# Kernel tuning notes

Hardware: AMD Instinct MI355X
Metric: run time of the kernel (lower is better)

The kernel has to match this reference:

```python
import jax, jax.numpy as jnp
import numpy as np

D_MODEL = 1024
NUM_HEADS = 16
D_IN = 1024

def setup_inputs() -> dict:
    key = jax.random.key(0)
    ks = jax.random.split(key, 5)
    scale = 1.0 / np.sqrt(D_IN)
    return {
        "in_features": jax.random.normal(ks[0], (4, 2048, D_IN), dtype=jnp.float32),
        "q_weight": jax.random.normal(ks[1], (D_MODEL, D_IN), dtype=jnp.float32) * scale,
        "k_weight": jax.random.normal(ks[2], (D_MODEL, D_IN), dtype=jnp.float32) * scale,
        "v_weight": jax.random.normal(ks[3], (D_MODEL, D_IN), dtype=jnp.float32) * scale,
        "o_weight": jax.random.normal(ks[4], (D_MODEL, D_MODEL), dtype=jnp.float32) * scale,
    }

def reference(in_features, q_weight, k_weight, v_weight, o_weight):
    batch, seq_len, _ = in_features.shape
    d_head = D_MODEL // NUM_HEADS
    # QKV projections (Linear with no bias: x @ W^T)
    q = jnp.einsum('bsi,di->bsd', in_features, q_weight)
    k = jnp.einsum('bsi,di->bsd', in_features, k_weight)
    v = jnp.einsum('bsi,di->bsd', in_features, v_weight)
    # split heads -> [b, h, s, d_head]
    q = q.reshape(batch, seq_len, NUM_HEADS, d_head).transpose(0, 2, 1, 3)
    k = k.reshape(batch, seq_len, NUM_HEADS, d_head).transpose(0, 2, 1, 3)
    v = v.reshape(batch, seq_len, NUM_HEADS, d_head).transpose(0, 2, 1, 3)
    # scaled dot-product attention (scale by per-head dim, as in SelfAttention)
    scores = jnp.einsum('bhqd,bhkd->bhqk', q, k) / jnp.sqrt(jnp.float32(d_head))
    probs = jax.nn.softmax(scores, axis=-1)
    ctx = jnp.einsum('bhqk,bhkd->bhqd', probs, v)
    # merge heads -> [b, s, d_model]
    ctx = ctx.transpose(0, 2, 1, 3).reshape(batch, seq_len, D_MODEL)
    # output projection
    return jnp.einsum('bsd,md->bsm', ctx, o_weight)
```

## Files before the change

kernel.cpp:

```cpp
#include <hip/hip_runtime.h>

typedef _Float16 half8 __attribute__((ext_vector_type(8)));
typedef _Float16 half4v __attribute__((ext_vector_type(4)));
typedef __fp16 fp16x2 __attribute__((ext_vector_type(2)));
typedef float f32x4 __attribute__((ext_vector_type(4)));
typedef float f32x16 __attribute__((ext_vector_type(16)));

__device__ __forceinline__ void gload_lds16(const _Float16* g, _Float16* l) {
    __builtin_amdgcn_global_load_lds(
        (const __attribute__((address_space(1))) void*)g,
        (__attribute__((address_space(3))) void*)l,
        16, 0, 0);
}

__global__ void cvt_f32_f16(const float* __restrict__ src, _Float16* __restrict__ dst, int n4) {
    int i = blockIdx.x * blockDim.x + threadIdx.x;
    if (i >= n4) return;
    f32x4 v = ((const f32x4*)src)[i];
    half4v h;
    h[0] = (_Float16)v[0]; h[1] = (_Float16)v[1];
    h[2] = (_Float16)v[2]; h[3] = (_Float16)v[3];
    ((half4v*)dst)[i] = h;
}

__global__ void cvt4_f32_f16(const float* __restrict__ s0, const float* __restrict__ s1,
                             const float* __restrict__ s2, const float* __restrict__ s3,
                             _Float16* __restrict__ dst) {
    int i = blockIdx.x * blockDim.x + threadIdx.x;
    int wsel = blockIdx.y;
    const float* src = (wsel == 0) ? s0 : (wsel == 1) ? s1 : (wsel == 2) ? s2 : s3;
    f32x4 v = ((const f32x4*)src)[i];
    half4v h;
    h[0] = (_Float16)v[0]; h[1] = (_Float16)v[1];
    h[2] = (_Float16)v[2]; h[3] = (_Float16)v[3];
    ((half4v*)(dst + (size_t)wsel * 1048576))[i] = h;
}

template<int MODE>
__global__ __launch_bounds__(256, 2)
void gemm_nt(const _Float16* __restrict__ A,
             const _Float16* __restrict__ Wbase,
             void* __restrict__ outbase)
{
    __shared__ _Float16 lds[32768];
    _Float16* Asb = lds;
    _Float16* Bsb = lds + 16384;

    const int tid  = threadIdx.x;
    const int lane = tid & 63;
    const int w    = tid >> 6;
    const int wr   = w >> 1, wc = w & 1;
    const int lr   = lane & 15, lg = lane >> 4;
    const int brow = blockIdx.x * 128;
    const int bcol = blockIdx.y * 128;
    const int mat  = (MODE == 0) ? blockIdx.z : 0;

    const _Float16* Ap = A + (size_t)brow * 1024;
    const _Float16* Bp = Wbase + (size_t)mat * (1024u * 1024u) + (size_t)bcol * 1024;

    const int srw  = tid >> 2;
    const int sch  = tid & 3;
    const int soff = ((sch ^ (srw & 3)) << 3);

    auto stage = [&](int buf, int kt) {
#pragma unroll
        for (int i = 0; i < 2; ++i) {
            const int ra = i * 64 + srw;
            gload_lds16(Ap + (size_t)ra * 1024 + kt * 32 + soff,
                        Asb + buf * 4096 + i * 2048 + w * 512);
            gload_lds16(Bp + (size_t)ra * 1024 + kt * 32 + soff,
                        Bsb + buf * 4096 + i * 2048 + w * 512);
        }
    };

    f32x4 acc[4][4] = {};
    const int swz = ((lg ^ (lr & 3)) << 3);

    stage(0, 0);
    stage(1, 1);
    asm volatile("s_waitcnt vmcnt(4)" ::: "memory");
    __builtin_amdgcn_s_barrier();
    __builtin_amdgcn_sched_barrier(0);

    for (int t = 0; t < 32; ++t) {
        if (t < 30) stage((t + 2) & 3, t + 2);
        const _Float16* Ab = Asb + (t & 3) * 4096;
        const _Float16* Bb = Bsb + (t & 3) * 4096;
        half8 af[4], bf[4];
#pragma unroll
        for (int mi = 0; mi < 4; ++mi)
            af[mi] = *(const half8*)&Ab[(wr * 64 + mi * 16 + lr) * 32 + swz];
#pragma unroll
        for (int ni = 0; ni < 4; ++ni)
            bf[ni] = *(const half8*)&Bb[(wc * 64 + ni * 16 + lr) * 32 + swz];
        __builtin_amdgcn_s_setprio(1);
#pragma unroll
        for (int mi = 0; mi < 4; ++mi)
#pragma unroll
            for (int ni = 0; ni < 4; ++ni)
                acc[mi][ni] = __builtin_amdgcn_mfma_f32_16x16x32_f16(af[mi], bf[ni], acc[mi][ni], 0, 0, 0);
        __builtin_amdgcn_s_setprio(0);
        if (t < 30)       { asm volatile("s_waitcnt vmcnt(4)" ::: "memory"); }
        else if (t == 30) { asm volatile("s_waitcnt vmcnt(0)" ::: "memory"); }
        if (t < 31) {
            __builtin_amdgcn_s_barrier();
            __builtin_amdgcn_sched_barrier(0);
        }
    }

    if (MODE == 0) {
        _Float16* outp = (_Float16*)outbase + (size_t)mat * (8192u * 1024u);
        if (mat == 2) {
            _Float16* Ts = lds;
#pragma unroll
            for (int p = 0; p < 2; ++p) {
                __syncthreads();
                if (wc == p) {
#pragma unroll
                    for (int mi = 0; mi < 4; ++mi)
#pragma unroll
                        for (int ni = 0; ni < 4; ++ni) {
                            int drow = ni * 16 + lr;
                            int s0   = wr * 64 + mi * 16 + lg * 4;
                            half4v o;
#pragma unroll
                            for (int r = 0; r < 4; ++r) o[r] = (_Float16)acc[mi][ni][r];
                            int byteoff = drow * 256 + s0 * 2;
                            byteoff ^= (drow & 7) << 4;
                            *(half4v*)((char*)Ts + byteoff) = o;
                        }
                }
                __syncthreads();
                {
                    int row   = tid >> 2;
                    int cbase = (tid & 3) * 4;
                    int gd = bcol + p * 64 + row;
                    int h = gd >> 6, dd = gd & 63;
                    int b = brow >> 11, sseq = brow & 2047;
                    _Float16* gout = outp + (((size_t)b * 16 + h) * 64 + dd) * 2048 + sseq;
#pragma unroll
                    for (int j = 0; j < 4; ++j) {
                        int c  = cbase + j;
                        int lc = c ^ (row & 7);
                        half8 v = *(const half8*)&Ts[row * 128 + lc * 8];
                        *(half8*)&gout[c * 8] = v;
                    }
                }
            }
        } else {
            const float scale = (mat == 0) ? 0.18033688f : 1.0f;
#pragma unroll
            for (int mi = 0; mi < 4; ++mi)
#pragma unroll
                for (int ni = 0; ni < 4; ++ni)
#pragma unroll
                    for (int r = 0; r < 4; ++r) {
                        int row = brow + wr * 64 + mi * 16 + lg * 4 + r;
                        int col = bcol + wc * 64 + ni * 16 + lr;
                        int b = row >> 11, s = row & 2047;
                        int h = col >> 6,  d = col & 63;
                        outp[(((size_t)b * 16 + h) * 2048 + s) * 64 + d] =
                            (_Float16)(acc[mi][ni][r] * scale);
                    }
        }
    } else {
        float* outp = (float*)outbase;
#pragma unroll
        for (int mi = 0; mi < 4; ++mi)
#pragma unroll
            for (int ni = 0; ni < 4; ++ni)
#pragma unroll
                for (int r = 0; r < 4; ++r) {
                    int row = brow + wr * 64 + mi * 16 + lg * 4 + r;
                    int col = bcol + wc * 64 + ni * 16 + lr;
                    outp[(size_t)row * 1024 + col] = acc[mi][ni][r];
                }
    }
}

#define M_FIX 10.0f
__global__ __launch_bounds__(256, 2)
void attn_kernel(const _Float16* __restrict__ Q,
                 const _Float16* __restrict__ Kx,
                 const _Float16* __restrict__ Vt,
                 _Float16* __restrict__ Ctx)
{
    __shared__ _Float16 Ks[2][64 * 72];
    __shared__ _Float16 Vs[2][64 * 72];

    const int tid = threadIdx.x, lane = tid & 63, w = tid >> 6;
    const int l31 = lane & 31, hi = lane >> 5;

    const int wg = blockIdx.x;
    const int j = ((wg & 7) << 6) + (wg >> 3);
    const int bh = j >> 3, qblk = j & 7;

    const _Float16* Qp  = Q  + ((size_t)bh * 2048 + qblk * 256) * 64;
    const _Float16* Kp  = Kx + (size_t)bh * 2048 * 64;
    const _Float16* Vtp = Vt + (size_t)bh * 64 * 2048;

    half8 qf[2][4];
#pragma unroll
    for (int g = 0; g < 2; ++g)
#pragma unroll
        for (int ks = 0; ks < 4; ++ks)
            qf[g][ks] = *(const half8*)(Qp + (size_t)(w * 64 + g * 32 + l31) * 64 + ks * 16 + hi * 8);

    const int srow = tid >> 3;
    const int scol = (tid & 7) * 8;
    const _Float16* Kg0 = Kp  + (size_t)srow * 64   + scol;
    const _Float16* Vg0 = Vtp + (size_t)srow * 2048 + scol;
    const int ldso = srow * 72 + scol;

    const fp16x2 ones2 = {(__fp16)1.0f, (__fp16)1.0f};

    f32x16 cacc[2][2] = {};
    float lp[2][2] = {};

    half8 kr0, kr1, vr0, vr1;
    kr0 = *(const half8*)(Kg0);
    kr1 = *(const half8*)(Kg0 + 2048);
    vr0 = *(const half8*)(Vg0);
    vr1 = *(const half8*)(Vg0 + 32 * 2048);
    *(half8*)&Ks[0][ldso]           = kr0;
    *(half8*)&Ks[0][ldso + 32 * 72] = kr1;
    *(half8*)&Vs[0][ldso]           = vr0;
    *(half8*)&Vs[0][ldso + 32 * 72] = vr1;
    __syncthreads();

    for (int t = 0; t < 32; ++t) {
        const int cur = t & 1;
        if (t < 31) {
            kr0 = *(const half8*)(Kg0 + (size_t)(t + 1) * 4096);
            kr1 = *(const half8*)(Kg0 + (size_t)(t + 1) * 4096 + 2048);
        }

        f32x16 sf[2][2];
        __builtin_amdgcn_s_setprio(1);
#pragma unroll
        for (int g = 0; g < 2; ++g)
#pragma unroll
            for (int kt = 0; kt < 2; ++kt) {
                f32x16 z;
#pragma unroll
                for (int r = 0; r < 16; ++r) z[r] = -M_FIX;
#pragma unroll
                for (int ks = 0; ks < 4; ++ks) {
                    half8 kf = *(const half8*)&Ks[cur][(kt * 32 + l31) * 72 + ks * 16 + hi * 8];
                    z = __builtin_amdgcn_mfma_f32_32x32x16_f16(kf, qf[g][ks], z, 0, 0, 0);
                }
                sf[g][kt] = z;
            }
        __builtin_amdgcn_s_setprio(0);

        if (t < 31) {
            *(half8*)&Ks[cur ^ 1][ldso]           = kr0;
            *(half8*)&Ks[cur ^ 1][ldso + 32 * 72] = kr1;
            vr0 = *(const half8*)(Vg0 + (t + 1) * 64);
            vr1 = *(const half8*)(Vg0 + (t + 1) * 64 + 32 * 2048);
        }

#pragma unroll
        for (int g = 0; g < 2; ++g) {
            half8 bf[4];
#pragma unroll
            for (int kt = 0; kt < 2; ++kt) {
#pragma unroll
                for (int r = 0; r < 16; ++r)
                    sf[g][kt][r] = __builtin_amdgcn_exp2f(sf[g][kt][r]);

                unsigned uq[4][2];
#pragma unroll
                for (int qd = 0; qd < 4; ++qd)
#pragma unroll
                    for (int w2 = 0; w2 < 2; ++w2)
                        uq[qd][w2] = __builtin_bit_cast(unsigned,
                            __builtin_amdgcn_cvt_pkrtz(sf[g][kt][4 * qd + 2 * w2],
                                                       sf[g][kt][4 * qd + 2 * w2 + 1]));

#pragma unroll
                for (int k1 = 0; k1 < 2; ++k1) {
                    union { half8 h; unsigned u[4]; } bu;
#pragma unroll
                    for (int w2 = 0; w2 < 2; ++w2) {
                        unsigned a = uq[2 * k1][w2];
                        unsigned b = uq[2 * k1 + 1][w2];
                        asm("v_permlane32_swap_b32 %0, %1" : "+v"(a), "+v"(b));
                        bu.u[w2]     = a;
                        bu.u[2 + w2] = b;
                    }
                    lp[g][0] = __builtin_amdgcn_fdot2(__builtin_bit_cast(fp16x2, bu.u[0]), ones2, lp[g][0], false);
                    lp[g][1] = __builtin_amdgcn_fdot2(__builtin_bit_cast(fp16x2, bu.u[1]), ones2, lp[g][1], false);
                    lp[g][0] = __builtin_amdgcn_fdot2(__builtin_bit_cast(fp16x2, bu.u[2]), ones2, lp[g][0], false);
                    lp[g][1] = __builtin_amdgcn_fdot2(__builtin_bit_cast(fp16x2, bu.u[3]), ones2, lp[g][1], false);
                    bf[kt * 2 + k1] = bu.h;
                }
            }

            __builtin_amdgcn_s_setprio(1);
#pragma unroll
            for (int dt = 0; dt < 2; ++dt)
#pragma unroll
                for (int ks = 0; ks < 4; ++ks) {
                    half8 vf = *(const half8*)&Vs[cur][(dt * 32 + l31) * 72 + ks * 16 + hi * 8];
                    cacc[g][dt] = __builtin_amdgcn_mfma_f32_32x32x16_f16(vf, bf[ks], cacc[g][dt], 0, 0, 0);
                }
            __builtin_amdgcn_s_setprio(0);
        }

        if (t < 31) {
            *(half8*)&Vs[cur ^ 1][ldso]           = vr0;
            *(half8*)&Vs[cur ^ 1][ldso + 32 * 72] = vr1;
        }
        __syncthreads();
    }

#pragma unroll
    for (int g = 0; g < 2; ++g) {
        float l = lp[g][0] + lp[g][1];
        const float inv = 1.0f / (l + __shfl_xor(l, 32, 64));
        const int s = qblk * 256 + w * 64 + g * 32 + l31;
        _Float16* Cp = Ctx + ((size_t)(bh >> 4) * 2048 + s) * 1024 + (bh & 15) * 64;
#pragma unroll
        for (int dt = 0; dt < 2; ++dt)
#pragma unroll
            for (int qd = 0; qd < 4; ++qd) {
                half4v o;
#pragma unroll
                for (int j2 = 0; j2 < 4; ++j2) o[j2] = (_Float16)(cacc[g][dt][4 * qd + j2] * inv);
                *(half4v*)&Cp[dt * 32 + qd * 8 + hi * 4] = o;
            }
    }
}

extern "C" void kernel_launch(void* const* d_in, const int* in_sizes, int n_in,
                              void* d_out, int out_size, void* d_ws, size_t ws_size,
                              hipStream_t stream)
{
    const float* X  = (const float*)d_in[0];
    const float* Wq = (const float*)d_in[1];
    const float* Wk = (const float*)d_in[2];
    const float* Wv = (const float*)d_in[3];
    const float* Wo = (const float*)d_in[4];

    if (ws_size < (size_t)(8 + 4 + 24) * 1024 * 1024 * 2) return;
    _Float16* Xh  = (_Float16*)d_ws;
    _Float16* Wh  = Xh + (size_t)8 * 1024 * 1024;
    _Float16* QKV = Wh + (size_t)4 * 1024 * 1024;
    _Float16* Ctx = Xh;

    cvt_f32_f16<<<8192, 256, 0, stream>>>(X, Xh, 2097152);
    cvt4_f32_f16<<<dim3(1024, 4), 256, 0, stream>>>(Wq, Wk, Wv, Wo, Wh);

    gemm_nt<0><<<dim3(64, 8, 3), 256, 0, stream>>>(Xh, Wh, QKV);

    attn_kernel<<<512, 256, 0, stream>>>(QKV, QKV + 8388608, QKV + 16777216, Ctx);

    gemm_nt<1><<<dim3(64, 8, 1), 256, 0, stream>>>(Ctx, Wh + 3145728, d_out);
}
```

Baseline: 188.7 us.

## Halve attention workgroup size to 128 threads and double grid to 1024 blocks

```diff
diff --git a/kernel.cpp b/kernel.cpp
--- a/kernel.cpp
+++ b/kernel.cpp
@@ -179,7 +179,7 @@
 }
 
 #define M_FIX 10.0f
-__global__ __launch_bounds__(256, 2)
+__global__ __launch_bounds__(128, 2)
 void attn_kernel(const _Float16* __restrict__ Q,
                  const _Float16* __restrict__ Kx,
                  const _Float16* __restrict__ Vt,
@@ -192,10 +192,10 @@
     const int l31 = lane & 31, hi = lane >> 5;
 
     const int wg = blockIdx.x;
-    const int j = ((wg & 7) << 6) + (wg >> 3);
-    const int bh = j >> 3, qblk = j & 7;
-
-    const _Float16* Qp  = Q  + ((size_t)bh * 2048 + qblk * 256) * 64;
+    const int j = ((wg & 7) << 7) + (wg >> 3);
+    const int bh = j >> 4, qblk = j & 15;
+
+    const _Float16* Qp  = Q  + ((size_t)bh * 2048 + qblk * 128) * 64;
     const _Float16* Kp  = Kx + (size_t)bh * 2048 * 64;
     const _Float16* Vtp = Vt + (size_t)bh * 64 * 2048;
 
@@ -217,22 +217,25 @@
     f32x16 cacc[2][2] = {};
     float lp[2][2] = {};
 
-    half8 kr0, kr1, vr0, vr1;
-    kr0 = *(const half8*)(Kg0);
-    kr1 = *(const half8*)(Kg0 + 2048);
-    vr0 = *(const half8*)(Vg0);
-    vr1 = *(const half8*)(Vg0 + 32 * 2048);
-    *(half8*)&Ks[0][ldso]           = kr0;
-    *(half8*)&Ks[0][ldso + 32 * 72] = kr1;
-    *(half8*)&Vs[0][ldso]           = vr0;
-    *(half8*)&Vs[0][ldso + 32 * 72] = vr1;
+    half8 kr[4], vr[4];
+#pragma unroll
+    for (int p = 0; p < 4; ++p) {
+        kr[p] = *(const half8*)(Kg0 + p * 1024);
+        vr[p] = *(const half8*)(Vg0 + p * 16 * 2048);
+    }
+#pragma unroll
+    for (int p = 0; p < 4; ++p) {
+        *(half8*)&Ks[0][ldso + p * 16 * 72] = kr[p];
+        *(half8*)&Vs[0][ldso + p * 16 * 72] = vr[p];
+    }
     __syncthreads();
 
     for (int t = 0; t < 32; ++t) {
         const int cur = t & 1;
         if (t < 31) {
-            kr0 = *(const half8*)(Kg0 + (size_t)(t + 1) * 4096);
-            kr1 = *(const half8*)(Kg0 + (size_t)(t + 1) * 4096 + 2048);
+#pragma unroll
+            for (int p = 0; p < 4; ++p)
+                kr[p] = *(const half8*)(Kg0 + (size_t)(t + 1) * 4096 + p * 1024);
         }
 
         f32x16 sf[2][2];
@@ -254,10 +257,12 @@
         __builtin_amdgcn_s_setprio(0);
 
         if (t < 31) {
-            *(half8*)&Ks[cur ^ 1][ldso]           = kr0;
-            *(half8*)&Ks[cur ^ 1][ldso + 32 * 72] = kr1;
-            vr0 = *(const half8*)(Vg0 + (t + 1) * 64);
-            vr1 = *(const half8*)(Vg0 + (t + 1) * 64 + 32 * 2048);
+#pragma unroll
+            for (int p = 0; p < 4; ++p)
+                *(half8*)&Ks[cur ^ 1][ldso + p * 16 * 72] = kr[p];
+#pragma unroll
+            for (int p = 0; p < 4; ++p)
+                vr[p] = *(const half8*)(Vg0 + (t + 1) * 64 + p * 16 * 2048);
         }
 
 #pragma unroll
@@ -309,8 +314,9 @@
         }
 
         if (t < 31) {
-            *(half8*)&Vs[cur ^ 1][ldso]           = vr0;
-            *(half8*)&Vs[cur ^ 1][ldso + 32 * 72] = vr1;
+#pragma unroll
+            for (int p = 0; p < 4; ++p)
+                *(half8*)&Vs[cur ^ 1][ldso + p * 16 * 72] = vr[p];
         }
         __syncthreads();
     }
@@ -319,7 +325,7 @@
     for (int g = 0; g < 2; ++g) {
         float l = lp[g][0] + lp[g][1];
         const float inv = 1.0f / (l + __shfl_xor(l, 32, 64));
-        const int s = qblk * 256 + w * 64 + g * 32 + l31;
+        const int s = qblk * 128 + w * 64 + g * 32 + l31;
         _Float16* Cp = Ctx + ((size_t)(bh >> 4) * 2048 + s) * 1024 + (bh & 15) * 64;
 #pragma unroll
         for (int dt = 0; dt < 2; ++dt)
@@ -354,7 +360,7 @@
 
     gemm_nt<0><<<dim3(64, 8, 3), 256, 0, stream>>>(Xh, Wh, QKV);
 
-    attn_kernel<<<512, 256, 0, stream>>>(QKV, QKV + 8388608, QKV + 16777216, Ctx);
+    attn_kernel<<<1024, 128, 0, stream>>>(QKV, QKV + 8388608, QKV + 16777216, Ctx);
 
     gemm_nt<1><<<dim3(64, 8, 1), 256, 0, stream>>>(Ctx, Wh + 3145728, d_out);
 }
```

After: 193.9 us. +2.8%, slower.
